# Optimization experiments

Hardware: AMD Instinct MI355X
Metric: run time of the kernel (lower is better)

Reference implementation:

```python
import jax, jax.numpy as jnp
import numpy as np

N = 100000      # nodes
E = 3200000     # directed edges (avg degree 32)
F_IN = 128      # node feature dim
H = 16          # hidden_features
A = 10          # num_actions


def setup_inputs() -> dict:
    key = jax.random.key(0)
    ks = jax.random.split(key, 8)
    x = jax.random.normal(ks[0], (N, F_IN), dtype=jnp.float32)
    edge_index = jax.random.randint(ks[1], (2, E), 0, N, dtype=jnp.int32)
    W1 = jax.random.normal(ks[2], (F_IN, H), dtype=jnp.float32) * (1.0 / np.sqrt(F_IN))
    b1 = jnp.zeros((H,), dtype=jnp.float32)
    W2 = jax.random.normal(ks[3], (H, H), dtype=jnp.float32) * (1.0 / np.sqrt(H))
    b2 = jnp.zeros((H,), dtype=jnp.float32)
    Wc = jax.random.normal(ks[4], (H, A), dtype=jnp.float32) * (1.0 / np.sqrt(H))
    bc = jnp.zeros((A,), dtype=jnp.float32)
    return {"x": x, "edge_index": edge_index, "W1": W1, "b1": b1,
            "W2": W2, "b2": b2, "Wc": Wc, "bc": bc}


def _gcn_norm(edge_index, n_nodes):
    # PyG GCNConv: add self-loops, symmetric normalization deg^-1/2 A_hat deg^-1/2
    loop = jnp.arange(n_nodes, dtype=edge_index.dtype)
    src = jnp.concatenate([edge_index[0], loop])   # message sources
    dst = jnp.concatenate([edge_index[1], loop])   # aggregation targets
    deg = jax.ops.segment_sum(jnp.ones_like(dst, dtype=jnp.float32), dst,
                              num_segments=n_nodes)
    dis = jnp.where(deg > 0, jax.lax.rsqrt(deg), 0.0)  # deg^-1/2, inf -> 0
    norm = dis[src] * dis[dst]                          # [E + N]
    return src, dst, norm


def _gcn_conv(h, W, b, src, dst, norm, n_nodes):
    # transform first (small output dim), then gather/scale/scatter-add
    msg = (h @ W)[src] * norm[:, None]                  # [E+N, out]
    return jax.ops.segment_sum(msg, dst, num_segments=n_nodes) + b


def reference(x, edge_index, W1, b1, W2, b2, Wc, bc):
    n_nodes = x.shape[0]
    src, dst, norm = _gcn_norm(edge_index, n_nodes)
    h = jax.nn.relu(_gcn_conv(x, W1, b1, src, dst, norm, n_nodes))
    # F.dropout(training=False) is identity at inference
    h = jax.nn.relu(_gcn_conv(h, W2, b2, src, dst, norm, n_nodes))
    pooled = jnp.max(h, axis=0)                         # global MaxAggregation -> [H]
    return pooled @ Wc + bc                             # squeeze() -> [A]
```

## Files before the change

kernel.cpp:

```cpp
#include <hip/hip_runtime.h>
#include <hip/hip_fp16.h>


#define FIN 128
#define HDIM 16
#define AOUT 10
#define NPB 256
#define KMAX 512
#define TILE 4096
#define CAP 10240

typedef _Float16 f16x8 __attribute__((ext_vector_type(8)));
typedef float f32x4 __attribute__((ext_vector_type(4)));

__global__ void k_init(int* __restrict__ bcur, unsigned int* __restrict__ pooled,
                       unsigned int* __restrict__ gza, unsigned int* __restrict__ gzb,
                       int K) {
    int i = blockIdx.x * 256 + threadIdx.x;
    if (i < K) bcur[i] = i * CAP;
    if (i < 16) pooled[i] = 0u;
    if (i < 8) { gza[i] = 0u; gzb[i] = 0u; }
}

__global__ __launch_bounds__(256) void k_bin(const int* __restrict__ src,
                                             const int* __restrict__ dst, int E,
                                             int* __restrict__ bcur,
                                             unsigned int* __restrict__ pairs, int K) {
    __shared__ int hist[KMAX], lofs[KMAX], run[KMAX], gbase[KMAX], ss[256];
    __shared__ unsigned int buf[TILE];
    __shared__ unsigned short bkt[TILE];
    int t = threadIdx.x;
    int e0 = blockIdx.x * TILE;
    int e1 = min(E, e0 + TILE);
    for (int i = t; i < KMAX; i += 256) hist[i] = 0;
    __syncthreads();
    for (int e = e0 + t * 4; e < e1; e += 1024) {
        if (e + 4 <= e1) {
            int4 d4 = *reinterpret_cast<const int4*>(dst + e);
            atomicAdd(&hist[d4.x >> 8], 1);
            atomicAdd(&hist[d4.y >> 8], 1);
            atomicAdd(&hist[d4.z >> 8], 1);
            atomicAdd(&hist[d4.w >> 8], 1);
        } else {
            for (int q = e; q < e1; q++) atomicAdd(&hist[dst[q] >> 8], 1);
        }
    }
    __syncthreads();
    int a0 = hist[2 * t], a1 = hist[2 * t + 1];
    int psum = a0 + a1;
    ss[t] = psum;
    for (int d = 1; d < 256; d <<= 1) {
        __syncthreads();
        int add = (t >= d) ? ss[t - d] : 0;
        __syncthreads();
        ss[t] += add;
    }
    __syncthreads();
    int excl = ss[t] - psum;
    lofs[2 * t] = excl;          run[2 * t] = excl;
    lofs[2 * t + 1] = excl + a0; run[2 * t + 1] = excl + a0;
    __syncthreads();
    for (int b = t; b < K; b += 256)
        if (hist[b]) gbase[b] = atomicAdd(&bcur[b], hist[b]);
    __syncthreads();
    for (int e = e0 + t * 4; e < e1; e += 1024) {
        if (e + 4 <= e1) {
            int4 d4 = *reinterpret_cast<const int4*>(dst + e);
            int4 s4 = *reinterpret_cast<const int4*>(src + e);
            int b, r;
            b = d4.x >> 8; r = atomicAdd(&run[b], 1);
            buf[r] = (unsigned)s4.x | ((unsigned)(d4.x & 255) << 17); bkt[r] = (unsigned short)b;
            b = d4.y >> 8; r = atomicAdd(&run[b], 1);
            buf[r] = (unsigned)s4.y | ((unsigned)(d4.y & 255) << 17); bkt[r] = (unsigned short)b;
            b = d4.z >> 8; r = atomicAdd(&run[b], 1);
            buf[r] = (unsigned)s4.z | ((unsigned)(d4.z & 255) << 17); bkt[r] = (unsigned short)b;
            b = d4.w >> 8; r = atomicAdd(&run[b], 1);
            buf[r] = (unsigned)s4.w | ((unsigned)(d4.w & 255) << 17); bkt[r] = (unsigned short)b;
        } else {
            for (int q = e; q < e1; q++) {
                int d = dst[q], s = src[q], b = d >> 8;
                int r = atomicAdd(&run[b], 1);
                buf[r] = (unsigned)s | ((unsigned)(d & 255) << 17);
                bkt[r] = (unsigned short)b;
            }
        }
    }
    __syncthreads();
    int m = e1 - e0;
    for (int i = t; i < m; i += 256) {
        int b = bkt[i];
        pairs[gbase[b] + i - lofs[b]] = buf[i];
    }
}

__global__ __launch_bounds__(512) void k_sort(const unsigned int* __restrict__ pairs,
                                              const int* __restrict__ bcur,
                                              int* __restrict__ srcidx,
                                              int2* __restrict__ off2,
                                              float* __restrict__ dis, int n) {
    __shared__ int lcnt[NPB], pre[NPB], cur[NPB];
    int b = blockIdx.x, t = threadIdx.x;
    if (t < NPB) lcnt[t] = 0;
    __syncthreads();
    int base = b * CAP;
    int m = bcur[b] - base;
    unsigned loc[20];
#pragma unroll
    for (int q = 0; q < 20; q++) {
        int j = t + q * 512;
        loc[q] = (j < m) ? pairs[base + j] : 0u;
        if (j < m) atomicAdd(&lcnt[loc[q] >> 17], 1);
    }
    __syncthreads();
    int v = (t < NPB) ? lcnt[t] : 0;
    int w = (v + 3) & ~3;
    if (t < NPB) pre[t] = w;
    for (int d = 1; d < NPB; d <<= 1) {
        __syncthreads();
        int add = (t < NPB && t >= d) ? pre[t - d] : 0;
        __syncthreads();
        if (t < NPB) pre[t] += add;
    }
    __syncthreads();
    if (t < NPB) {
        int start = pre[t] - w;
        cur[t] = start;
        int node = (b << 8) + t;
        if (node < n) {
            off2[node] = make_int2(base + start, base + start + v);
            dis[node] = rsqrtf((float)(v + 1));
        }
        for (int p = v; p < w; p++) srcidx[base + start + p] = n;
    }
    __syncthreads();
#pragma unroll
    for (int q = 0; q < 20; q++) {
        int j = t + q * 512;
        if (j < m) {
            unsigned p = loc[q];
            int pos = base + atomicAdd(&cur[p >> 17], 1);
            srcidx[pos] = (int)(p & 0x1FFFF);
        }
    }
}

__global__ __launch_bounds__(256) void k_gemm1(const float* __restrict__ x,
                                               const float* __restrict__ W1,
                                               const float* __restrict__ dis,
                                               __half* __restrict__ g16, int n) {
    int l = threadIdx.x & 63;
    int cc = l & 15, kg = l >> 4;
    f16x8 bfrag[4];
#pragma unroll
    for (int kc = 0; kc < 4; kc++)
#pragma unroll
        for (int j = 0; j < 8; j++)
            bfrag[kc][j] = (_Float16)W1[(kc * 32 + kg * 8 + j) * HDIM + cc];
    int tile = blockIdx.x * 4 + (threadIdx.x >> 6);
    int node0 = tile * 16;
    if (node0 >= n) return;
    const float* xr = x + (size_t)(node0 + cc) * FIN;
    f32x4 acc = {0.f, 0.f, 0.f, 0.f};
#pragma unroll
    for (int kc = 0; kc < 4; kc++) {
        float4 xa = *reinterpret_cast<const float4*>(xr + kc * 32 + kg * 8);
        float4 xb = *reinterpret_cast<const float4*>(xr + kc * 32 + kg * 8 + 4);
        f16x8 a;
        a[0] = (_Float16)xa.x; a[1] = (_Float16)xa.y;
        a[2] = (_Float16)xa.z; a[3] = (_Float16)xa.w;
        a[4] = (_Float16)xb.x; a[5] = (_Float16)xb.y;
        a[6] = (_Float16)xb.z; a[7] = (_Float16)xb.w;
        acc = __builtin_amdgcn_mfma_f32_16x16x32_f16(a, bfrag[kc], acc, 0, 0, 0);
    }
#pragma unroll
    for (int i = 0; i < 4; i++) {
        int nd = node0 + kg * 4 + i;
        g16[(size_t)nd * HDIM + cc] = (__half)(dis[nd] * acc[i]);
    }
}

#define ACC4(V) \
    a0 = __hadd2(a0, __builtin_bit_cast(__half2, (V).x)); \
    a1 = __hadd2(a1, __builtin_bit_cast(__half2, (V).y)); \
    a2 = __hadd2(a2, __builtin_bit_cast(__half2, (V).z)); \
    a3 = __hadd2(a3, __builtin_bit_cast(__half2, (V).w));

#define GATHER_LOOP \
    int e = e0 + 4 * half; \
    for (; e + 8 < e1; e += 16) { \
        int4 sa = *reinterpret_cast<const int4*>(srcidx + e); \
        int4 sb = *reinterpret_cast<const int4*>(srcidx + e + 8); \
        uint4 w0 = gp[(size_t)sa.x * 2 + piece]; \
        uint4 w1 = gp[(size_t)sa.y * 2 + piece]; \
        uint4 w2 = gp[(size_t)sa.z * 2 + piece]; \
        uint4 w3 = gp[(size_t)sa.w * 2 + piece]; \
        uint4 w4 = gp[(size_t)sb.x * 2 + piece]; \
        uint4 w5 = gp[(size_t)sb.y * 2 + piece]; \
        uint4 w6 = gp[(size_t)sb.z * 2 + piece]; \
        uint4 w7 = gp[(size_t)sb.w * 2 + piece]; \
        ACC4(w0) ACC4(w1) ACC4(w2) ACC4(w3) \
        ACC4(w4) ACC4(w5) ACC4(w6) ACC4(w7) \
    } \
    for (; e < e1; e += 8) { \
        int4 sa = *reinterpret_cast<const int4*>(srcidx + e); \
        uint4 w0 = gp[(size_t)sa.x * 2 + piece]; \
        uint4 w1 = gp[(size_t)sa.y * 2 + piece]; \
        uint4 w2 = gp[(size_t)sa.z * 2 + piece]; \
        uint4 w3 = gp[(size_t)sa.w * 2 + piece]; \
        ACC4(w0) ACC4(w1) ACC4(w2) ACC4(w3) \
    } \
    a0 = __hadd2(a0, __builtin_bit_cast(__half2, __shfl_xor(__builtin_bit_cast(unsigned, a0), 2))); \
    a1 = __hadd2(a1, __builtin_bit_cast(__half2, __shfl_xor(__builtin_bit_cast(unsigned, a1), 2))); \
    a2 = __hadd2(a2, __builtin_bit_cast(__half2, __shfl_xor(__builtin_bit_cast(unsigned, a2), 2))); \
    a3 = __hadd2(a3, __builtin_bit_cast(__half2, __shfl_xor(__builtin_bit_cast(unsigned, a3), 2)));

__global__ __launch_bounds__(256) void k_agg_g2(const __half* __restrict__ g16in,
                                                const int2* __restrict__ off2,
                                                const int* __restrict__ srcidx,
                                                const float* __restrict__ dis,
                                                const float* __restrict__ bias,
                                                const float* __restrict__ W2,
                                                __half* __restrict__ g16out, int n) {
    __shared__ float W2s[HDIM * HDIM];
    int t = threadIdx.x;
    W2s[t] = W2[t];
    __syncthreads();
    int tid = blockIdx.x * 256 + t;
    int node = tid >> 2, sub = t & 3;
    int piece = sub & 1, half = sub >> 1;
    if (node >= n) return;
    const uint4* gp = reinterpret_cast<const uint4*>(g16in);
    int2 oe = off2[node];
    int e0 = oe.x, e1 = oe.y;
    __half2 a0{0, 0}, a1{0, 0}, a2{0, 0}, a3{0, 0};
    if (half == 0) {
        uint4 v = gp[(size_t)node * 2 + piece];
        ACC4(v)
    }
    GATHER_LOOP
    float dn = dis[node];
    const float* bp = bias + piece * 8;
    float2 f0 = __half22float2(a0), f1 = __half22float2(a1);
    float2 f2 = __half22float2(a2), f3 = __half22float2(a3);
    float hreg[8];
    hreg[0] = fmaxf(dn * f0.x + bp[0], 0.f); hreg[1] = fmaxf(dn * f0.y + bp[1], 0.f);
    hreg[2] = fmaxf(dn * f1.x + bp[2], 0.f); hreg[3] = fmaxf(dn * f1.y + bp[3], 0.f);
    hreg[4] = fmaxf(dn * f2.x + bp[4], 0.f); hreg[5] = fmaxf(dn * f2.y + bp[5], 0.f);
    hreg[6] = fmaxf(dn * f3.x + bp[6], 0.f); hreg[7] = fmaxf(dn * f3.y + bp[7], 0.f);
    float acc[8];
    const float* wq = W2s + (piece * 8) * HDIM + half * 8;
#pragma unroll
    for (int cc = 0; cc < 8; cc++) {
        float s = 0.f;
#pragma unroll
        for (int jj = 0; jj < 8; jj++) s += hreg[jj] * wq[jj * HDIM + cc];
        acc[cc] = s;
    }
#pragma unroll
    for (int cc = 0; cc < 8; cc++) acc[cc] += __shfl_xor(acc[cc], 1);
    if (piece == 0) {
        __half o[8];
#pragma unroll
        for (int cc = 0; cc < 8; cc++) o[cc] = (__half)(dn * acc[cc]);
        *reinterpret_cast<uint4*>(g16out + (size_t)node * HDIM + half * 8) =
            *reinterpret_cast<uint4*>(o);
    }
}

__global__ __launch_bounds__(256) void k_agg_pool(const __half* __restrict__ g16in,
                                                  const int2* __restrict__ off2,
                                                  const int* __restrict__ srcidx,
                                                  const float* __restrict__ dis,
                                                  const float* __restrict__ bias,
                                                  unsigned int* __restrict__ pooled,
                                                  int n) {
    __shared__ float smax[4][16];
    int t = threadIdx.x;
    int tid = blockIdx.x * 256 + t;
    int node = tid >> 2, sub = t & 3;
    int piece = sub & 1, half = sub >> 1;
    bool active = node < n;
    float4 o0 = {0.f, 0.f, 0.f, 0.f}, o1 = {0.f, 0.f, 0.f, 0.f};
    if (active) {
        const uint4* gp = reinterpret_cast<const uint4*>(g16in);
        int2 oe = off2[node];
        int e0 = oe.x, e1 = oe.y;
        __half2 a0{0, 0}, a1{0, 0}, a2{0, 0}, a3{0, 0};
        if (half == 0) {
            uint4 v = gp[(size_t)node * 2 + piece];
            ACC4(v)
        }
        GATHER_LOOP
        if (half == 0) {
            float dn = dis[node];
            const float* bp = bias + piece * 8;
            float2 f0 = __half22float2(a0), f1 = __half22float2(a1);
            float2 f2 = __half22float2(a2), f3 = __half22float2(a3);
            o0.x = fmaxf(dn * f0.x + bp[0], 0.f); o0.y = fmaxf(dn * f0.y + bp[1], 0.f);
            o0.z = fmaxf(dn * f1.x + bp[2], 0.f); o0.w = fmaxf(dn * f1.y + bp[3], 0.f);
            o1.x = fmaxf(dn * f2.x + bp[4], 0.f); o1.y = fmaxf(dn * f2.y + bp[5], 0.f);
            o1.z = fmaxf(dn * f3.x + bp[6], 0.f); o1.w = fmaxf(dn * f3.y + bp[7], 0.f);
        }
    }
#pragma unroll
    for (int d = 4; d <= 32; d <<= 1) {
        o0.x = fmaxf(o0.x, __shfl_xor(o0.x, d)); o0.y = fmaxf(o0.y, __shfl_xor(o0.y, d));
        o0.z = fmaxf(o0.z, __shfl_xor(o0.z, d)); o0.w = fmaxf(o0.w, __shfl_xor(o0.w, d));
        o1.x = fmaxf(o1.x, __shfl_xor(o1.x, d)); o1.y = fmaxf(o1.y, __shfl_xor(o1.y, d));
        o1.z = fmaxf(o1.z, __shfl_xor(o1.z, d)); o1.w = fmaxf(o1.w, __shfl_xor(o1.w, d));
    }
    int wv = t >> 6;
    if ((t & 63) < 2) {
        float* sp = &smax[wv][piece * 8];
        sp[0] = o0.x; sp[1] = o0.y; sp[2] = o0.z; sp[3] = o0.w;
        sp[4] = o1.x; sp[5] = o1.y; sp[6] = o1.z; sp[7] = o1.w;
    }
    __syncthreads();
    if (t < 16) {
        float m = fmaxf(fmaxf(smax[0][t], smax[1][t]), fmaxf(smax[2][t], smax[3][t]));
        atomicMax(&pooled[t], __float_as_uint(m));
    }
}

__global__ void k_final(const unsigned int* __restrict__ pooled, const float* __restrict__ Wc,
                        const float* __restrict__ bc, float* __restrict__ out) {
    __shared__ float p[HDIM];
    int t = threadIdx.x;
    if (t < HDIM) p[t] = __uint_as_float(pooled[t]);
    __syncthreads();
    if (t < AOUT) {
        float acc = bc[t];
#pragma unroll
        for (int c = 0; c < HDIM; c++) acc += p[c] * Wc[c * AOUT + t];
        out[t] = acc;
    }
}

extern "C" void kernel_launch(void* const* d_in, const int* in_sizes, int n_in,
                              void* d_out, int out_size, void* d_ws, size_t ws_size,
                              hipStream_t stream) {
    const float* x  = (const float*)d_in[0];
    const int*   ei = (const int*)d_in[1];
    const float* W1 = (const float*)d_in[2];
    const float* b1 = (const float*)d_in[3];
    const float* W2 = (const float*)d_in[4];
    const float* b2 = (const float*)d_in[5];
    const float* Wc = (const float*)d_in[6];
    const float* bc = (const float*)d_in[7];
    float* out = (float*)d_out;

    int n = in_sizes[0] / FIN;
    int E = in_sizes[1] / 2;
    const int* srcp = ei;
    const int* dstp = ei + E;
    int K = (n + NPB - 1) / NPB;

    char* ws = (char*)d_ws;
    auto alloc = [&](size_t bytes) -> char* {
        char* p = ws;
        ws += (bytes + 255) & ~(size_t)255;
        return p;
    };
    float*        dis   = (float*)alloc((size_t)n * 4);
    int*          bcur  = (int*)alloc((size_t)K * 4);
    int2*         off2  = (int2*)alloc((size_t)n * 8);
    unsigned int* pairs = (unsigned int*)alloc((size_t)K * CAP * 4);
    int*          srcidx= (int*)alloc((size_t)K * CAP * 4);
    __half*       g16a  = (__half*)alloc((size_t)(n + 1) * HDIM * 2);
    __half*       g16b  = (__half*)alloc((size_t)(n + 1) * HDIM * 2);
    unsigned int* pooled= (unsigned int*)alloc(64);

    k_init<<<(K + 255) / 256, 256, 0, stream>>>(
        bcur, pooled,
        (unsigned int*)(g16a + (size_t)n * HDIM),
        (unsigned int*)(g16b + (size_t)n * HDIM), K);
    k_bin<<<(E + TILE - 1) / TILE, 256, 0, stream>>>(srcp, dstp, E, bcur, pairs, K);
    k_sort<<<K, 512, 0, stream>>>(pairs, bcur, srcidx, off2, dis, n);

    int ntile = (n + 15) / 16;
    int gblocks = (ntile + 3) / 4;
    k_gemm1<<<gblocks, 256, 0, stream>>>(x, W1, dis, g16a, n);
    k_agg_g2<<<(4 * n + 255) / 256, 256, 0, stream>>>(g16a, off2, srcidx, dis, b1,
                                                      W2, g16b, n);
    k_agg_pool<<<(4 * n + 255) / 256, 256, 0, stream>>>(g16b, off2, srcidx, dis, b2,
                                                        pooled, n);

    k_final<<<1, 64, 0, stream>>>(pooled, Wc, bc, out);
}
```

Before: 131.4 us.

## Stage dst in LDS, widen sort blocks, fuse final matvec into pooling

Three separate changes. k_bin now keeps its tile of dst indices in shared memory during the histogram pass, so the scatter pass does not read dst from global memory again. k_sort runs 1024 threads per bucket block instead of 512, which halves the per-thread register array. The final classifier kernel is removed, and the last block of k_agg_pool, found with a done counter and threadfence, does the pooled@Wc+bc itself, saving one launch. The cost is 16KB more LDS per k_bin block, which may lower occupancy, plus an extra atomic per pooling block.

```diff
diff --git a/kernel.cpp b/kernel.cpp
--- a/kernel.cpp
+++ b/kernel.cpp
@@ -15,11 +15,12 @@
 
 __global__ void k_init(int* __restrict__ bcur, unsigned int* __restrict__ pooled,
                        unsigned int* __restrict__ gza, unsigned int* __restrict__ gzb,
-                       int K) {
+                       unsigned int* __restrict__ done, int K) {
     int i = blockIdx.x * 256 + threadIdx.x;
     if (i < K) bcur[i] = i * CAP;
     if (i < 16) pooled[i] = 0u;
     if (i < 8) { gza[i] = 0u; gzb[i] = 0u; }
+    if (i == 0) *done = 0u;
 }
 
 __global__ __launch_bounds__(256) void k_bin(const int* __restrict__ src,
@@ -27,6 +28,7 @@
                                              int* __restrict__ bcur,
                                              unsigned int* __restrict__ pairs, int K) {
     __shared__ int hist[KMAX], lofs[KMAX], run[KMAX], gbase[KMAX], ss[256];
+    __shared__ int stage_d[TILE];
     __shared__ unsigned int buf[TILE];
     __shared__ unsigned short bkt[TILE];
     int t = threadIdx.x;
@@ -35,14 +37,20 @@
     for (int i = t; i < KMAX; i += 256) hist[i] = 0;
     __syncthreads();
     for (int e = e0 + t * 4; e < e1; e += 1024) {
+        int li = e - e0;
         if (e + 4 <= e1) {
             int4 d4 = *reinterpret_cast<const int4*>(dst + e);
+            *reinterpret_cast<int4*>(stage_d + li) = d4;
             atomicAdd(&hist[d4.x >> 8], 1);
             atomicAdd(&hist[d4.y >> 8], 1);
             atomicAdd(&hist[d4.z >> 8], 1);
             atomicAdd(&hist[d4.w >> 8], 1);
         } else {
-            for (int q = e; q < e1; q++) atomicAdd(&hist[dst[q] >> 8], 1);
+            for (int q = e; q < e1; q++) {
+                int d = dst[q];
+                stage_d[q - e0] = d;
+                atomicAdd(&hist[d >> 8], 1);
+            }
         }
     }
     __syncthreads();
@@ -64,8 +72,9 @@
         if (hist[b]) gbase[b] = atomicAdd(&bcur[b], hist[b]);
     __syncthreads();
     for (int e = e0 + t * 4; e < e1; e += 1024) {
+        int li = e - e0;
         if (e + 4 <= e1) {
-            int4 d4 = *reinterpret_cast<const int4*>(dst + e);
+            int4 d4 = *reinterpret_cast<const int4*>(stage_d + li);
             int4 s4 = *reinterpret_cast<const int4*>(src + e);
             int b, r;
             b = d4.x >> 8; r = atomicAdd(&run[b], 1);
@@ -78,7 +87,7 @@
             buf[r] = (unsigned)s4.w | ((unsigned)(d4.w & 255) << 17); bkt[r] = (unsigned short)b;
         } else {
             for (int q = e; q < e1; q++) {
-                int d = dst[q], s = src[q], b = d >> 8;
+                int d = stage_d[q - e0], s = src[q], b = d >> 8;
                 int r = atomicAdd(&run[b], 1);
                 buf[r] = (unsigned)s | ((unsigned)(d & 255) << 17);
                 bkt[r] = (unsigned short)b;
@@ -93,21 +102,21 @@
     }
 }
 
-__global__ __launch_bounds__(512) void k_sort(const unsigned int* __restrict__ pairs,
-                                              const int* __restrict__ bcur,
-                                              int* __restrict__ srcidx,
-                                              int2* __restrict__ off2,
-                                              float* __restrict__ dis, int n) {
+__global__ __launch_bounds__(1024) void k_sort(const unsigned int* __restrict__ pairs,
+                                               const int* __restrict__ bcur,
+                                               int* __restrict__ srcidx,
+                                               int2* __restrict__ off2,
+                                               float* __restrict__ dis, int n) {
     __shared__ int lcnt[NPB], pre[NPB], cur[NPB];
     int b = blockIdx.x, t = threadIdx.x;
     if (t < NPB) lcnt[t] = 0;
     __syncthreads();
     int base = b * CAP;
     int m = bcur[b] - base;
-    unsigned loc[20];
-#pragma unroll
-    for (int q = 0; q < 20; q++) {
-        int j = t + q * 512;
+    unsigned loc[10];
+#pragma unroll
+    for (int q = 0; q < 10; q++) {
+        int j = t + q * 1024;
         loc[q] = (j < m) ? pairs[base + j] : 0u;
         if (j < m) atomicAdd(&lcnt[loc[q] >> 17], 1);
     }
@@ -134,8 +143,8 @@
     }
     __syncthreads();
 #pragma unroll
-    for (int q = 0; q < 20; q++) {
-        int j = t + q * 512;
+    for (int q = 0; q < 10; q++) {
+        int j = t + q * 1024;
         if (j < m) {
             unsigned p = loc[q];
             int pos = base + atomicAdd(&cur[p >> 17], 1);
@@ -273,8 +282,13 @@
                                                   const float* __restrict__ dis,
                                                   const float* __restrict__ bias,
                                                   unsigned int* __restrict__ pooled,
-                                                  int n) {
+                                                  unsigned int* __restrict__ done,
+                                                  const float* __restrict__ Wc,
+                                                  const float* __restrict__ bc,
+                                                  float* __restrict__ out, int n) {
     __shared__ float smax[4][16];
+    __shared__ unsigned int islast;
+    __shared__ float pP[HDIM];
     int t = threadIdx.x;
     int tid = blockIdx.x * 256 + t;
     int node = tid >> 2, sub = t & 3;
@@ -320,19 +334,19 @@
         float m = fmaxf(fmaxf(smax[0][t], smax[1][t]), fmaxf(smax[2][t], smax[3][t]));
         atomicMax(&pooled[t], __float_as_uint(m));
     }
-}
-
-__global__ void k_final(const unsigned int* __restrict__ pooled, const float* __restrict__ Wc,
-                        const float* __restrict__ bc, float* __restrict__ out) {
-    __shared__ float p[HDIM];
-    int t = threadIdx.x;
-    if (t < HDIM) p[t] = __uint_as_float(pooled[t]);
-    __syncthreads();
-    if (t < AOUT) {
-        float acc = bc[t];
-#pragma unroll
-        for (int c = 0; c < HDIM; c++) acc += p[c] * Wc[c * AOUT + t];
-        out[t] = acc;
+    __syncthreads();
+    __threadfence();
+    if (t == 0) islast = (atomicAdd(done, 1u) == gridDim.x - 1) ? 1u : 0u;
+    __syncthreads();
+    if (islast) {
+        if (t < HDIM) pP[t] = __uint_as_float(atomicMax(&pooled[t], 0u));
+        __syncthreads();
+        if (t < AOUT) {
+            float acc = bc[t];
+#pragma unroll
+            for (int c = 0; c < HDIM; c++) acc += pP[c] * Wc[c * AOUT + t];
+            out[t] = acc;
+        }
     }
 }
 
@@ -369,13 +383,14 @@
     __half*       g16a  = (__half*)alloc((size_t)(n + 1) * HDIM * 2);
     __half*       g16b  = (__half*)alloc((size_t)(n + 1) * HDIM * 2);
     unsigned int* pooled= (unsigned int*)alloc(64);
+    unsigned int* done  = (unsigned int*)alloc(64);
 
     k_init<<<(K + 255) / 256, 256, 0, stream>>>(
         bcur, pooled,
         (unsigned int*)(g16a + (size_t)n * HDIM),
-        (unsigned int*)(g16b + (size_t)n * HDIM), K);
+        (unsigned int*)(g16b + (size_t)n * HDIM), done, K);
     k_bin<<<(E + TILE - 1) / TILE, 256, 0, stream>>>(srcp, dstp, E, bcur, pairs, K);
-    k_sort<<<K, 512, 0, stream>>>(pairs, bcur, srcidx, off2, dis, n);
+    k_sort<<<K, 1024, 0, stream>>>(pairs, bcur, srcidx, off2, dis, n);
 
     int ntile = (n + 15) / 16;
     int gblocks = (ntile + 3) / 4;
@@ -383,7 +398,5 @@
     k_agg_g2<<<(4 * n + 255) / 256, 256, 0, stream>>>(g16a, off2, srcidx, dis, b1,
                                                       W2, g16b, n);
     k_agg_pool<<<(4 * n + 255) / 256, 256, 0, stream>>>(g16b, off2, srcidx, dis, b2,
-                                                        pooled, n);
-
-    k_final<<<1, 64, 0, stream>>>(pooled, Wc, bc, out);
-}
+                                                        pooled, done, Wc, bc, out, n);
+}
```

New measurement: 239.3 us. 82.1% more time.
